# Optimization experiments

Measured on AMD Instinct MI355X. Metric: run time of the kernel, lower is better.

Reference implementation:

```python
import jax, jax.numpy as jnp
import numpy as np
from jax import lax

B, C, H, W = 1, 256, 64, 64
A = 9            # number of anchor sizes
STRIDE = 16      # base_stride
G = 28           # roi_grid_size
POOL = G // 2    # after 2x2 max pool -> 14
KPRE = 2000      # proposals entering NMS (obj_rank)
KPOST = 256      # RoIs kept after NMS
NCLS = 21        # head classes; head out dim = 5*NCLS
IOU_THR = 0.7


def _anchors():
    r = 2.0 ** 0.5
    out = []
    for b in (128.0, 256.0, 512.0):
        out += [(b, b), (b * r, b / r), (b / r, b * r)]
    return np.asarray(out, np.float32)  # [A,2] = (h, w)


def setup_inputs() -> dict:
    key = jax.random.key(0)
    ks = jax.random.split(key, 6)
    x = jax.random.normal(ks[0], (B, C, H, W), jnp.float32)
    rpn_w = jax.random.normal(ks[1], (256, C, 3, 3), jnp.float32) * 0.02
    rpn_b = jnp.zeros((256,), jnp.float32)
    cls_w = jax.random.normal(ks[2], (2 * A, 256), jnp.float32) * 0.05
    cls_b = jnp.zeros((2 * A,), jnp.float32)
    tfm_w = jax.random.normal(ks[3], (4 * A, 256), jnp.float32) * 0.01
    tfm_b = jnp.zeros((4 * A,), jnp.float32)
    head_w = jax.random.normal(ks[4], (5 * NCLS, C * POOL * POOL), jnp.float32) * 0.01
    head_b = jnp.zeros((5 * NCLS,), jnp.float32)
    anchors = jnp.asarray(_anchors())
    return dict(x=x, rpn_w=rpn_w, rpn_b=rpn_b, cls_w=cls_w, cls_b=cls_b,
                tfm_w=tfm_w, tfm_b=tfm_b, head_w=head_w, head_b=head_b,
                anchors=anchors)


def _forward(x, rpn_w, rpn_b, cls_w, cls_b, tfm_w, tfm_b, head_w, head_b, anchors):
    fm = x  # base == identity: input IS the backbone feature map [B,C,H,W]
    h = lax.conv_general_dilated(fm, rpn_w, (1, 1), 'SAME',
                                 dimension_numbers=('NCHW', 'OIHW', 'NCHW'))
    h = h + rpn_b[None, :, None, None]
    rpn_cls = jnp.einsum('oc,bchw->bohw', cls_w, h) + cls_b[None, :, None, None]
    rpn_tfm = jnp.einsum('oc,bchw->bohw', tfm_w, h) + tfm_b[None, :, None, None]

    # objectness: exp(pos)/(exp(pos)+exp(neg)) == sigmoid(pos-neg); channels interleaved
    obj = jax.nn.sigmoid(rpn_cls[:, 0::2] - rpn_cls[:, 1::2])  # [B,A,H,W]

    t = rpn_tfm.reshape(B, A, 4, H, W)
    aw = anchors[:, 1][None, :, None, None]
    ah = anchors[:, 0][None, :, None, None]
    jj = jnp.arange(W, dtype=jnp.float32)[None, None, None, :]
    ii = jnp.arange(H, dtype=jnp.float32)[None, None, :, None]
    bx = jj + aw * (t[:, :, 1] - 0.5) / STRIDE
    by = ii + ah * (t[:, :, 0] - 0.5) / STRIDE
    bw = aw / STRIDE * jnp.exp(t[:, :, 3])
    bh = ah / STRIDE * jnp.exp(t[:, :, 2])
    bx = jnp.clip(bx, 0.0, W - 1.0)
    by = jnp.clip(by, 0.0, H - 1.0)
    bw = jnp.clip(bx + bw, 0.0, W - 1.0) - bx
    bh = jnp.clip(by + bh, 0.0, H - 1.0) - by

    score = obj.reshape(-1)  # B==1, all scores > 0 (matches obj_score.nonzero())
    top_s, idx = lax.top_k(score, KPRE)  # sort descending (proposal ranking)
    # proposal path is computed under no_grad in the original
    top_s = lax.stop_gradient(top_s)
    bx, by, bw, bh = [lax.stop_gradient(v.reshape(-1)[idx]) for v in (bx, by, bw, bh)]

    # pairwise IoU on (x,y,w,h) boxes
    x2 = bx + bw; y2 = by + bh; area = bw * bh
    ix = jnp.maximum(bx[:, None], bx[None, :])
    iy = jnp.maximum(by[:, None], by[None, :])
    iw = jnp.clip(jnp.minimum(x2[:, None], x2[None, :]) - ix, 0.0)
    ih = jnp.clip(jnp.minimum(y2[:, None], y2[None, :]) - iy, 0.0)
    inter = iw * ih
    iou = inter / (area[:, None] + area[None, :] - inter)

    ar = jnp.arange(KPRE)
    def body(i, keep):  # greedy sequential NMS over score-sorted proposals
        sup = (iou[i] > IOU_THR) & (ar > i) & keep[i]
        return keep & (~sup)
    keep = lax.fori_loop(0, KPRE, body, jnp.ones((KPRE,), bool))

    _, sel = lax.top_k(jnp.where(keep, top_s, 0.0), KPOST)
    rx, ry, rw, rh = bx[sel], by[sel], bw[sel], bh[sel]  # feature-map coords

    fm0 = fm[0]  # [C,H,W]
    def align(px, py, pw, ph):
        # 28x28 bilinear sampling grid over the RoI, then 2x2 max pool -> 14x14
        gx = jnp.clip(px + (jnp.arange(G, dtype=jnp.float32) + 0.5) * pw / G, 0.0, W - 1.0)
        gy = jnp.clip(py + (jnp.arange(G, dtype=jnp.float32) + 0.5) * ph / G, 0.0, H - 1.0)
        x0 = jnp.clip(jnp.floor(gx), 0, W - 2).astype(jnp.int32)
        y0 = jnp.clip(jnp.floor(gy), 0, H - 2).astype(jnp.int32)
        wx = (gx - x0)[None, None, :]
        wy = (gy - y0)[None, :, None]
        f00 = fm0[:, y0[:, None], x0[None, :]]
        f01 = fm0[:, y0[:, None] + 1, x0[None, :]]
        f10 = fm0[:, y0[:, None], x0[None, :] + 1]
        f11 = fm0[:, y0[:, None] + 1, x0[None, :] + 1]
        out = (f00 * (1 - wy) * (1 - wx) + f01 * wy * (1 - wx)
               + f10 * (1 - wy) * wx + f11 * wy * wx)  # [C,G,G]
        return out.reshape(C, POOL, 2, POOL, 2).max(axis=(2, 4))

    feats = jax.vmap(align)(rx, ry, rw, rh)              # [KPOST,C,14,14]
    head_out = feats.reshape(KPOST, -1) @ head_w.T + head_b  # [KPOST,5*NCLS]
    final_cls = head_out[:, :NCLS]
    final_tfm = head_out[:, NCLS:]
    det = jnp.argmax(final_cls, axis=1)
    k = jnp.arange(KPOST)
    t0 = final_tfm[k, det * 4]
    t1 = final_tfm[k, det * 4 + 1]
    t2 = final_tfm[k, det * 4 + 2]
    t3 = final_tfm[k, det * 4 + 3]

    X = rx * STRIDE; Y = ry * STRIDE; Wd = rw * STRIDE; Hd = rh * STRIDE  # image coords
    fx = X + Wd * t1
    fy = Y + Hd * t0
    fw = Wd * jnp.exp(t3)
    fh = Hd * jnp.exp(t2)
    img = jnp.zeros((KPOST,), jnp.float32)
    final_bbox = jnp.stack([img, fx, fy, fw, fh], axis=1)
    proposal_bbox = jnp.stack([img, X, Y, Wd, Hd], axis=1)
    return rpn_cls, rpn_tfm, proposal_bbox, final_bbox, final_cls, final_tfm


def reference(x, rpn_w, rpn_b, cls_w, cls_b, tfm_w, tfm_b, head_w, head_b, anchors):
    return _forward(x, rpn_w, rpn_b, cls_w, cls_b, tfm_w, tfm_b, head_w, head_b, anchors)
```

## Files before the change

### kernel.cpp

```cpp
#include <hip/hip_runtime.h>
#include <math.h>

#define NPX   4096
#define NSC   36864
#define NKPRE 2000
#define NKPOST 256
#define GKS   98
#define CSPL  4

#define F_HPART  0
#define F_PART   0
#define F_H      4194304
#define F_FMT    5242880
#define F_XBH    6291456
#define F_XBL    6849024
#define F_WBH    7406592
#define F_WBL    7701504
#define F_FEATSB 6291456
#define F_HWB    12713984
#define F_UKEY   15523840
#define F_BX     15560704
#define F_BY     15597568
#define F_BW     15634432
#define F_BH     15671296
#define F_HIST   15708160
#define F_CAND   15773696
#define F_MASK   15781888
#define F_RBX    15909888
#define F_RBY    15911888
#define F_RBW    15913888
#define F_RBH    15915888
#define F_SEL    15917888
#define F_RXS    15918144
#define F_RYS    15918400
#define F_RWS    15918656
#define F_RHS    15918912
#define F_META   15919168
#define F_PRANK  15919184

typedef unsigned long long u64;
typedef unsigned int u32;
typedef unsigned short ushort;
typedef __attribute__((ext_vector_type(8))) short short8;
typedef __attribute__((ext_vector_type(4))) float floatx4;

__device__ __forceinline__ ushort f2bf(float f) {
    u32 b = __float_as_uint(f);
    b += 0x7FFFu + ((b >> 16) & 1u);
    return (ushort)(b >> 16);
}
__device__ __forceinline__ float bf2f(ushort h) {
    return __uint_as_float(((u32)h) << 16);
}
__device__ __forceinline__ u64 RL64(u64 v, int l) {
    u32 lo = (u32)__builtin_amdgcn_readlane((int)(u32)v, l);
    u32 hi = (u32)__builtin_amdgcn_readlane((int)(u32)(v >> 32), l);
    return ((u64)hi << 32) | lo;
}

__global__ void k_init(int* __restrict__ hist, int* __restrict__ meta,
                       int* __restrict__ prank) {
    int i = blockIdx.x * 256 + threadIdx.x;
    if (i < 65536) hist[i] = 0;
    if (i < 16) meta[i] = 0;
    if (i < 4096) prank[i] = 0;
}

__global__ void k_hwb(const float* __restrict__ head_w, ushort* __restrict__ hwb) {
    int e = (blockIdx.x * 256 + threadIdx.x) * 4;
    int o = e / 50176, k = e % 50176;
    ushort4 r;
    if (o < 105) {
        float4 v = *(const float4*)(head_w + (size_t)o * 50176 + k);
        r.x = f2bf(v.x); r.y = f2bf(v.y); r.z = f2bf(v.z); r.w = f2bf(v.w);
    } else {
        r.x = r.y = r.z = r.w = 0;
    }
    *(ushort4*)(hwb + (size_t)o * 50176 + k) = r;
}

__global__ void __launch_bounds__(256) k_transpose(const float* __restrict__ x,
                                                   float* __restrict__ fmt) {
    __shared__ float t[64][65];
    int pt = blockIdx.x;
    int ct = blockIdx.y;
    int tid = threadIdx.x;
    int px0 = pt * 64, c0 = ct * 64;
    int ln = tid & 63, sub = tid >> 6;
    for (int p = 0; p < 16; ++p) {
        int cl = p * 4 + sub;
        t[ln][cl] = x[(c0 + cl) * 4096 + px0 + ln];
    }
    __syncthreads();
    for (int p = 0; p < 16; ++p) {
        int pl = p * 4 + sub;
        fmt[(px0 + pl) * 256 + c0 + ln] = t[pl][ln];
    }
}

__global__ void k_xb(const float* __restrict__ fmt, ushort* __restrict__ xbh,
                     ushort* __restrict__ xbl) {
    int e = blockIdx.x * 256 + threadIdx.x;
    int p = e >> 6, cq = (e & 63) * 4;
    int yy = p / 66, xx = p % 66;
    float4 v = {0.f, 0.f, 0.f, 0.f};
    if (yy >= 1 && yy <= 64 && xx >= 1 && xx <= 64)
        v = *(const float4*)&fmt[((yy - 1) * 64 + (xx - 1)) * 256 + cq];
    ushort4 h, l;
    h.x = f2bf(v.x); l.x = f2bf(v.x - bf2f(h.x));
    h.y = f2bf(v.y); l.y = f2bf(v.y - bf2f(h.y));
    h.z = f2bf(v.z); l.z = f2bf(v.z - bf2f(h.z));
    h.w = f2bf(v.w); l.w = f2bf(v.w - bf2f(h.w));
    *(ushort4*)&xbh[(size_t)p * 256 + cq] = h;
    *(ushort4*)&xbl[(size_t)p * 256 + cq] = l;
}

__global__ void k_wb(const float* __restrict__ rpn_w, ushort* __restrict__ wbh,
                     ushort* __restrict__ wbl) {
    int e = blockIdx.x * 256 + threadIdx.x;
    int c = e & 255, oc = (e >> 8) & 255, t = e >> 16;
    float v = rpn_w[oc * 2304 + c * 9 + t];
    ushort h = f2bf(v);
    wbh[e] = h;
    wbl[e] = f2bf(v - bf2f(h));
}

__global__ void __launch_bounds__(256) k_conv(const ushort* __restrict__ xbh,
        const ushort* __restrict__ xbl, const ushort* __restrict__ wbh,
        const ushort* __restrict__ wbl, float* __restrict__ hpart) {
    __shared__ ushort lah[64 * 40], lal[64 * 40];
    __shared__ ushort lbh[64 * 40], lbl[64 * 40];
    int y0 = blockIdx.x;
    int oc0 = blockIdx.y * 64;
    int ksp = blockIdx.z;
    int tid = threadIdx.x;
    int wave = tid >> 6, lane = tid & 63;
    int m16 = lane & 15, quad = lane >> 4;
    floatx4 acc[4];
    #pragma unroll
    for (int nt = 0; nt < 4; ++nt) acc[nt] = (floatx4){0.f, 0.f, 0.f, 0.f};
    int sr = tid >> 2, sch = (tid & 3) * 8;
    for (int ki = ksp * 18; ki < ksp * 18 + 18; ++ki) {
        int t = ki >> 3, cb = ki & 7;
        int dy = t / 3, dx = t % 3;
        __syncthreads();
        {
            int rA0 = (y0 + dy) * 66 + dx;
            size_t g = (size_t)(rA0 + sr) * 256 + cb * 32 + sch;
            *(short8*)&lah[sr * 40 + sch] = *(const short8*)&xbh[g];
            *(short8*)&lal[sr * 40 + sch] = *(const short8*)&xbl[g];
        }
        {
            size_t g = (size_t)t * 65536 + (size_t)(oc0 + sr) * 256 + cb * 32 + sch;
            *(short8*)&lbh[sr * 40 + sch] = *(const short8*)&wbh[g];
            *(short8*)&lbl[sr * 40 + sch] = *(const short8*)&wbl[g];
        }
        __syncthreads();
        short8 ah = *(const short8*)&lah[(wave * 16 + m16) * 40 + quad * 8];
        short8 al = *(const short8*)&lal[(wave * 16 + m16) * 40 + quad * 8];
        #pragma unroll
        for (int nt = 0; nt < 4; ++nt) {
            short8 bh = *(const short8*)&lbh[(nt * 16 + m16) * 40 + quad * 8];
            short8 bl = *(const short8*)&lbl[(nt * 16 + m16) * 40 + quad * 8];
            acc[nt] = __builtin_amdgcn_mfma_f32_16x16x32_bf16(al, bh, acc[nt], 0, 0, 0);
            acc[nt] = __builtin_amdgcn_mfma_f32_16x16x32_bf16(ah, bl, acc[nt], 0, 0, 0);
            acc[nt] = __builtin_amdgcn_mfma_f32_16x16x32_bf16(ah, bh, acc[nt], 0, 0, 0);
        }
    }
    float* hp = hpart + (size_t)ksp * 1048576;
    #pragma unroll
    for (int nt = 0; nt < 4; ++nt) {
        int oc = oc0 + nt * 16 + m16;
        #pragma unroll
        for (int reg = 0; reg < 4; ++reg) {
            int px = y0 * 64 + wave * 16 + quad * 4 + reg;
            hp[oc * 4096 + px] = acc[nt][reg];
        }
    }
}

__global__ void k_convreduce(const float* __restrict__ hpart,
                             const float* __restrict__ rpn_b,
                             float* __restrict__ h) {
    int e = blockIdx.x * 256 + threadIdx.x;
    float s = 0.f;
    #pragma unroll
    for (int k = 0; k < CSPL; ++k) s += hpart[(size_t)k * 1048576 + e];
    h[e] = s + rpn_b[e >> 12];
}

__global__ void __launch_bounds__(256) k_heads(const float* __restrict__ h,
        const float* __restrict__ cls_w, const float* __restrict__ cls_b,
        const float* __restrict__ tfm_w, const float* __restrict__ tfm_b,
        const float* __restrict__ anchors,
        float* __restrict__ out_cls, float* __restrict__ out_tfm,
        u32* __restrict__ ukey, float* __restrict__ bxp, float* __restrict__ byp,
        float* __restrict__ bwp, float* __restrict__ bhp, int* __restrict__ hist) {
    __shared__ float w[256 * 56];
    __shared__ float ds[32 * 55];
    int tid = threadIdx.x;
    int px0 = blockIdx.x * 32;
    for (int e = tid; e < 54 * 256; e += 256) {
        int o = e >> 8, c = e & 255;
        float v = (o < 18) ? cls_w[o * 256 + c] : tfm_w[(o - 18) * 256 + c];
        w[c * 56 + o] = v;
    }
    __syncthreads();
    int ploc = tid & 31, og = tid >> 5;
    int px = px0 + ploc;
    float acc[7];
    #pragma unroll
    for (int j = 0; j < 7; ++j) acc[j] = 0.f;
    for (int c = 0; c < 256; ++c) {
        float hv = h[c * 4096 + px];
        #pragma unroll
        for (int j = 0; j < 7; ++j) acc[j] += hv * w[c * 56 + og * 7 + j];
    }
    #pragma unroll
    for (int j = 0; j < 7; ++j) {
        int o = og * 7 + j;
        if (o < 54) {
            float b = (o < 18) ? cls_b[o] : tfm_b[o - 18];
            float val = acc[j] + b;
            if (o < 18) out_cls[o * 4096 + px] = val;
            else        out_tfm[(o - 18) * 4096 + px] = val;
            ds[ploc * 55 + o] = val;
        }
    }
    __syncthreads();
    for (int t = tid; t < 288; t += 256) {
        int a = t >> 5, p = t & 31;
        int pxx = px0 + p;
        float pos = ds[p * 55 + 2 * a];
        float neg = ds[p * 55 + 2 * a + 1];
        float d = pos - neg;
        float sc = 1.f / (1.f + expf(-d));
        float t0 = ds[p * 55 + 18 + 4 * a + 0];
        float t1 = ds[p * 55 + 18 + 4 * a + 1];
        float t2 = ds[p * 55 + 18 + 4 * a + 2];
        float t3 = ds[p * 55 + 18 + 4 * a + 3];
        float ah = anchors[a * 2 + 0], aw = anchors[a * 2 + 1];
        float jx = (float)(pxx & 63), iy = (float)(pxx >> 6);
        float bx = jx + aw * (t1 - 0.5f) / 16.f;
        float by = iy + ah * (t0 - 0.5f) / 16.f;
        float bw = aw / 16.f * expf(t3);
        float bh = ah / 16.f * expf(t2);
        bx = fminf(fmaxf(bx, 0.f), 63.f);
        by = fminf(fmaxf(by, 0.f), 63.f);
        bw = fminf(fmaxf(bx + bw, 0.f), 63.f) - bx;
        bh = fminf(fmaxf(by + bh, 0.f), 63.f) - by;
        int idx = a * 4096 + pxx;
        u32 bits = __float_as_uint(sc);
        u32 u = (bits & 0x80000000u) ? ~bits : (bits ^ 0x80000000u);
        ukey[idx] = u;
        bxp[idx] = bx; byp[idx] = by; bwp[idx] = bw; bhp[idx] = bh;
        atomicAdd(&hist[u >> 16], 1);
    }
}

__global__ void __launch_bounds__(1024) k_scan(const int* __restrict__ hist,
                                               int* __restrict__ meta) {
    __shared__ int s[1024];
    int t = threadIdx.x;
    int base = 65536 - 64 * (t + 1);
    int sum = 0;
    for (int i = 0; i < 64; ++i) sum += hist[base + i];
    s[t] = sum;
    __syncthreads();
    int own = sum;
    for (int off = 1; off < 1024; off <<= 1) {
        int v = (t >= off) ? s[t - off] : 0;
        __syncthreads();
        s[t] += v;
        __syncthreads();
    }
    int cum = s[t], prev = cum - own;
    if (prev < NKPRE && cum >= NKPRE) {
        int c = prev;
        int b = 65535 - 64 * t;
        for (int i = 0; i < 64; ++i) {
            c += hist[b - i];
            if (c >= NKPRE) { meta[0] = b - i; break; }
        }
    }
}

__global__ void k_compact(const u32* __restrict__ ukey, const int* __restrict__ meta,
                          u64* __restrict__ cand, int* __restrict__ cnt) {
    int i = blockIdx.x * 256 + threadIdx.x;
    if (i >= NSC) return;
    u32 u = ukey[i];
    if ((int)(u >> 16) >= meta[0]) {
        int pos = atomicAdd(cnt, 1);
        if (pos < 4096) cand[pos] = (((u64)(~u)) << 32) | (u32)i;
    }
}

__global__ void __launch_bounds__(256) k_rank(const u64* __restrict__ cand,
                                              int* __restrict__ prank) {
    __shared__ u64 sk[256];
    int tid = threadIdx.x;
    int i = blockIdx.x * 256 + tid;
    int j0 = blockIdx.y * 256;
    sk[tid] = cand[j0 + tid];
    __syncthreads();
    u64 mykey = cand[i];
    int r = 0;
    #pragma unroll 8
    for (int j = 0; j < 256; j += 2) {
        ulonglong2 kv = *(const ulonglong2*)&sk[j];
        r += (kv.x < mykey) ? 1 : 0;
        r += (kv.y < mykey) ? 1 : 0;
    }
    atomicAdd(&prank[i], r);
}

__global__ void k_place(const u64* __restrict__ cand, const int* __restrict__ meta,
        const int* __restrict__ prank,
        const float* __restrict__ bxp, const float* __restrict__ byp,
        const float* __restrict__ bwp, const float* __restrict__ bhp,
        float* __restrict__ rbx, float* __restrict__ rby,
        float* __restrict__ rbw, float* __restrict__ rbh) {
    int i = blockIdx.x * 256 + threadIdx.x;
    int vc = meta[1]; if (vc > 4096) vc = 4096;
    if (i >= vc) return;
    int r = prank[i];
    if (r >= NKPRE) return;
    int idx = (int)(u32)(cand[i] & 0xFFFFFFFFULL);
    rbx[r] = bxp[idx]; rby[r] = byp[idx]; rbw[r] = bwp[idx]; rbh[r] = bhp[idx];
}

__global__ void __launch_bounds__(256) k_mask(const float* __restrict__ rbx,
        const float* __restrict__ rby, const float* __restrict__ rbw,
        const float* __restrict__ rbh, u64* __restrict__ mask) {
    int i = blockIdx.x;
    int lane = threadIdx.x & 63;
    int wave = threadIdx.x >> 6;
    float bxi = rbx[i], byi = rby[i], bwi = rbw[i], bhi = rbh[i];
    float x2i = bxi + bwi, y2i = byi + bhi, ari = bwi * bhi;
    for (int w = wave; w < 32; w += 4) {
        int j = w * 64 + lane;
        bool p = false;
        if (j < NKPRE && j > i) {
            float bxj = rbx[j], byj = rby[j], bwj = rbw[j], bhj = rbh[j];
            float x2j = bxj + bwj, y2j = byj + bhj, arj = bwj * bhj;
            float ix = fmaxf(bxi, bxj), iy = fmaxf(byi, byj);
            float iw = fmaxf(fminf(x2i, x2j) - ix, 0.f);
            float ih = fmaxf(fminf(y2i, y2j) - iy, 0.f);
            float inter = iw * ih;
            float iou = inter / (ari + arj - inter);
            p = iou > 0.7f;
        }
        u64 b = __ballot(p);
        if (lane == 0) mask[i * 32 + w] = b;
    }
}

__global__ void __launch_bounds__(64) k_nms(const u64* __restrict__ mask,
        const float* __restrict__ rbx, const float* __restrict__ rby,
        const float* __restrict__ rbw, const float* __restrict__ rbh,
        int* __restrict__ sel, float* __restrict__ rxs, float* __restrict__ rys,
        float* __restrict__ rws, float* __restrict__ rhs,
        u64* __restrict__ scratch) {
    __shared__ int klist[256];
    int lane = threadIdx.x;
    int lw = lane & 31;
    {
        const ulonglong2* m2 = (const ulonglong2*)mask;
        u64 acc = 0;
        #pragma unroll 25
        for (int it = lane; it < 32000; it += 64) {
            ulonglong2 v = m2[it];
            acc |= v.x | v.y;
        }
        scratch[lane] = acc;
    }
    u64 removed = 0ULL;
    int kcount = 0;
    u64 pf[32];
    #pragma unroll
    for (int s = 0; s < 32; ++s) pf[s] = mask[s * 32 + lw];
    bool done = false;
    for (int ib = 0; ib < NKPRE; ib += 32) {
        if (done) break;
        int cw = ib >> 6;
        int iw = (ib + 32) >> 6;
        u64 remC = RL64(removed, cw);
        u64 remI = RL64(removed, iw);
        #pragma unroll
        for (int s = 0; s < 32; ++s) {
            int ii = ib + s;
            u64 row = pf[s];
            int nx = ii + 32;
            if (!done && nx < NKPRE && !((remI >> (nx & 63)) & 1ULL))
                pf[s] = mask[(size_t)nx * 32 + lw];
            if (!done && ii < NKPRE && !((remC >> (ii & 63)) & 1ULL)) {
                if (lane == 0) klist[kcount] = ii;
                kcount++;
                if (lane < 32) removed |= row;
                remC |= RL64(row, cw);
                remI |= RL64(row, iw);
                if (kcount == NKPOST) done = true;
            }
        }
    }
    if (kcount < NKPOST) {
        for (int w = 0; w < 32 && kcount < NKPOST; ++w) {
            u64 wv = RL64(removed, w);
            int base = w << 6;
            for (int b = 0; b < 64; ++b) {
                int ii = base + b;
                if (ii >= NKPRE || kcount >= NKPOST) break;
                if ((wv >> b) & 1ULL) {
                    if (lane == 0) klist[kcount] = ii;
                    kcount++;
                }
            }
        }
    }
    __syncthreads();
    for (int s = lane; s < NKPOST; s += 64) {
        int id = klist[s];
        sel[s] = id;
        rxs[s] = rbx[id]; rys[s] = rby[id]; rws[s] = rbw[id]; rhs[s] = rbh[id];
    }
}

__global__ void __launch_bounds__(256) k_align(const float* __restrict__ fmt,
        const float* __restrict__ rxs, const float* __restrict__ rys,
        const float* __restrict__ rws, const float* __restrict__ rhs,
        ushort* __restrict__ feats) {
    __shared__ float buf[64 * 99];
    __shared__ int xs0[28], ys0[28];
    __shared__ float wxs[28], wys[28];
    int roi = blockIdx.x;
    int c0 = blockIdx.y * 64;
    int ch0 = blockIdx.z * 98;
    int tid = threadIdx.x;
    float rx = rxs[roi], ry = rys[roi], rw = rws[roi], rh = rhs[roi];
    if (tid < 28) {
        float g = rx + ((float)tid + 0.5f) * rw / 28.f;
        g = fminf(fmaxf(g, 0.f), 63.f);
        int x0 = (int)floorf(g); x0 = min(max(x0, 0), 62);
        xs0[tid] = x0; wxs[tid] = g - (float)x0;
        float g2 = ry + ((float)tid + 0.5f) * rh / 28.f;
        g2 = fminf(fmaxf(g2, 0.f), 63.f);
        int y0 = (int)floorf(g2); y0 = min(max(y0, 0), 62);
        ys0[tid] = y0; wys[tid] = g2 - (float)y0;
    }
    __syncthreads();
    int cl = tid & 63, cg = tid >> 6;
    for (int l = cg; l < 98; l += 4) {
        int cell = ch0 + l;
        int py = cell / 14, pxc = cell % 14;
        float m = -INFINITY;
        #pragma unroll
        for (int dy = 0; dy < 2; ++dy) {
            int sy = py * 2 + dy;
            int y0 = ys0[sy]; float wy = wys[sy];
            #pragma unroll
            for (int dx = 0; dx < 2; ++dx) {
                int sx = pxc * 2 + dx;
                int x0 = xs0[sx]; float wx = wxs[sx];
                int base = (y0 * 64 + x0) * 256 + c0 + cl;
                float f00 = fmt[base];
                float f10 = fmt[base + 256];
                float f01 = fmt[base + 64 * 256];
                float f11 = fmt[base + 64 * 256 + 256];
                float v = f00 * (1.f - wy) * (1.f - wx) + f01 * wy * (1.f - wx)
                        + f10 * (1.f - wy) * wx + f11 * wy * wx;
                m = fmaxf(m, v);
            }
        }
        buf[cl * 99 + l] = m;
    }
    __syncthreads();
    for (int e = tid; e < 64 * 98; e += 256) {
        int c = e / 98, l = e % 98;
        feats[(size_t)roi * 50176 + (c0 + c) * 196 + ch0 + l] = f2bf(buf[c * 99 + l]);
    }
}

__global__ void __launch_bounds__(256) k_gemm(const ushort* __restrict__ fb,
        const ushort* __restrict__ hwb, float* __restrict__ part) {
    int ks = blockIdx.x, rt = blockIdx.y;
    int wave = threadIdx.x >> 6, lane = threadIdx.x & 63;
    int m16 = lane & 15, quad = lane >> 4;
    int roiBase = rt * 64 + wave * 16;
    int kb = ks * 512;
    const ushort* arow = fb + (size_t)(roiBase + m16) * 50176 + kb + quad * 8;
    const ushort* brow = hwb + (size_t)m16 * 50176 + kb + quad * 8;
    floatx4 acc[7];
    #pragma unroll
    for (int t = 0; t < 7; ++t) acc[t] = (floatx4){0.f, 0.f, 0.f, 0.f};
    #pragma unroll 4
    for (int step = 0; step < 16; ++step) {
        short8 a = *(const short8*)(arow + step * 32);
        #pragma unroll
        for (int t = 0; t < 7; ++t) {
            short8 b = *(const short8*)(brow + (size_t)t * 16 * 50176 + step * 32);
            acc[t] = __builtin_amdgcn_mfma_f32_16x16x32_bf16(a, b, acc[t], 0, 0, 0);
        }
    }
    float* pbase = part + (size_t)ks * 26880;
    #pragma unroll
    for (int t = 0; t < 7; ++t) {
        int o = t * 16 + m16;
        if (o < 105) {
            #pragma unroll
            for (int reg = 0; reg < 4; ++reg) {
                int roi = roiBase + quad * 4 + reg;
                pbase[roi * 105 + o] = acc[t][reg];
            }
        }
    }
}

__global__ void k_reduce(const float* __restrict__ part, const float* __restrict__ head_b,
                         float* __restrict__ out_cls, float* __restrict__ out_tfm) {
    int e = blockIdx.x * 256 + threadIdx.x;
    if (e >= 26880) return;
    int roi = e / 105, o = e % 105;
    float s = 0.f;
    for (int ks = 0; ks < GKS; ++ks) s += part[(size_t)ks * 26880 + e];
    s += head_b[o];
    if (o < 21) out_cls[roi * 21 + o] = s;
    else        out_tfm[roi * 84 + (o - 21)] = s;
}

__global__ void __launch_bounds__(256) k_final(const float* __restrict__ out_cls,
        const float* __restrict__ out_tfm,
        const float* __restrict__ rxs, const float* __restrict__ rys,
        const float* __restrict__ rws, const float* __restrict__ rhs,
        float* __restrict__ prop, float* __restrict__ fbox) {
    int r = threadIdx.x;
    float best = out_cls[r * 21]; int det = 0;
    for (int o = 1; o < 21; ++o) {
        float v = out_cls[r * 21 + o];
        if (v > best) { best = v; det = o; }
    }
    float t0 = out_tfm[r * 84 + det * 4 + 0];
    float t1 = out_tfm[r * 84 + det * 4 + 1];
    float t2 = out_tfm[r * 84 + det * 4 + 2];
    float t3 = out_tfm[r * 84 + det * 4 + 3];
    float X = rxs[r] * 16.f, Y = rys[r] * 16.f, Wd = rws[r] * 16.f, Hd = rhs[r] * 16.f;
    float fx = X + Wd * t1, fy = Y + Hd * t0;
    float fw = Wd * expf(t3), fh = Hd * expf(t2);
    prop[r * 5 + 0] = 0.f; prop[r * 5 + 1] = X;  prop[r * 5 + 2] = Y;
    prop[r * 5 + 3] = Wd;  prop[r * 5 + 4] = Hd;
    fbox[r * 5 + 0] = 0.f; fbox[r * 5 + 1] = fx; fbox[r * 5 + 2] = fy;
    fbox[r * 5 + 3] = fw;  fbox[r * 5 + 4] = fh;
}

extern "C" void kernel_launch(void* const* d_in, const int* in_sizes, int n_in,
                              void* d_out, int out_size, void* d_ws, size_t ws_size,
                              hipStream_t stream) {
    const float* x      = (const float*)d_in[0];
    const float* rpn_w  = (const float*)d_in[1];
    const float* rpn_b  = (const float*)d_in[2];
    const float* cls_w  = (const float*)d_in[3];
    const float* cls_b  = (const float*)d_in[4];
    const float* tfm_w  = (const float*)d_in[5];
    const float* tfm_b  = (const float*)d_in[6];
    const float* head_w = (const float*)d_in[7];
    const float* head_b = (const float*)d_in[8];
    const float* anch   = (const float*)d_in[9];
    float* out = (float*)d_out;
    float* ws  = (float*)d_ws;

    float*  hpart  = ws + F_HPART;
    float*  h      = ws + F_H;
    float*  fmt    = ws + F_FMT;
    ushort* xbh    = (ushort*)(ws + F_XBH);
    ushort* xbl    = (ushort*)(ws + F_XBL);
    ushort* wbh    = (ushort*)(ws + F_WBH);
    ushort* wbl    = (ushort*)(ws + F_WBL);
    ushort* featsb = (ushort*)(ws + F_FEATSB);
    ushort* hwb    = (ushort*)(ws + F_HWB);
    float*  part   = ws + F_PART;
    u32*    ukey   = (u32*)(ws + F_UKEY);
    float*  bxp    = ws + F_BX;
    float*  byp    = ws + F_BY;
    float*  bwp    = ws + F_BW;
    float*  bhp    = ws + F_BH;
    int*    hist   = (int*)(ws + F_HIST);
    u64*    cand   = (u64*)(ws + F_CAND);
    u64*    mask   = (u64*)(ws + F_MASK);
    float*  rbx    = ws + F_RBX;
    float*  rby    = ws + F_RBY;
    float*  rbw    = ws + F_RBW;
    float*  rbh    = ws + F_RBH;
    int*    sel    = (int*)(ws + F_SEL);
    float*  rxs    = ws + F_RXS;
    float*  rys    = ws + F_RYS;
    float*  rws_p  = ws + F_RWS;
    float*  rhs_p  = ws + F_RHS;
    int*    meta   = (int*)(ws + F_META);
    int*    prank  = (int*)(ws + F_PRANK);

    float* out_rpncls = out + 0;
    float* out_rpntfm = out + 73728;
    float* out_prop   = out + 221184;
    float* out_fbox   = out + 222464;
    float* out_fcls   = out + 223744;
    float* out_ftfm   = out + 229120;

    k_init<<<256, 256, 0, stream>>>(hist, meta, prank);
    k_hwb<<<5488, 256, 0, stream>>>(head_w, hwb);
    k_transpose<<<dim3(64, 4), 256, 0, stream>>>(x, fmt);
    k_xb<<<1089, 256, 0, stream>>>(fmt, xbh, xbl);
    k_wb<<<2304, 256, 0, stream>>>(rpn_w, wbh, wbl);
    k_conv<<<dim3(64, 4, 4), 256, 0, stream>>>(xbh, xbl, wbh, wbl, hpart);
    k_convreduce<<<4096, 256, 0, stream>>>(hpart, rpn_b, h);
    k_heads<<<128, 256, 0, stream>>>(h, cls_w, cls_b, tfm_w, tfm_b, anch,
                                     out_rpncls, out_rpntfm, ukey, bxp, byp, bwp, bhp, hist);
    k_scan<<<1, 1024, 0, stream>>>(hist, meta);
    k_compact<<<144, 256, 0, stream>>>(ukey, meta, cand, meta + 1);
    k_rank<<<dim3(16, 16), 256, 0, stream>>>(cand, prank);
    k_place<<<16, 256, 0, stream>>>(cand, meta, prank, bxp, byp, bwp, bhp,
                                    rbx, rby, rbw, rbh);
    k_mask<<<2000, 256, 0, stream>>>(rbx, rby, rbw, rbh, mask);
    k_nms<<<1, 64, 0, stream>>>(mask, rbx, rby, rbw, rbh, sel, rxs, rys, rws_p, rhs_p,
                                cand);
    k_align<<<dim3(256, 4, 2), 256, 0, stream>>>(fmt, rxs, rys, rws_p, rhs_p, featsb);
    k_gemm<<<dim3(98, 4), 256, 0, stream>>>(featsb, hwb, part);
    k_reduce<<<105, 256, 0, stream>>>(part, head_b, out_fcls, out_ftfm);
    k_final<<<1, 256, 0, stream>>>(out_fcls, out_ftfm, rxs, rys, rws_p, rhs_p,
                                   out_prop, out_fbox);
}
```

Measured before the change: 343.8 us.

## Restructure NMS selection scan to per-64-box word processing with ctz iteration

Replaces the serial per-box greedy NMS scan, which kept 32 prefetched mask rows in registers and checked every box, with a per-64-box word loop. Each lane holds its diagonal mask word, the kept boxes inside a word are found by ctz iteration over the alive bits, and only kept rows are then loaded to update the removed set. The fill-up path for padding suppressed boxes now uses a wave-wide ballot-like popcount prefix instead of a serial bit loop. This cuts the iterations spent on suppressed boxes and the register pressure, but adds a readlane per kept box and serial dependent loads of kept rows.

```diff
diff --git a/kernel.cpp b/kernel.cpp
--- a/kernel.cpp
+++ b/kernel.cpp
@@ -377,45 +377,51 @@
     }
     u64 removed = 0ULL;
     int kcount = 0;
-    u64 pf[32];
-    #pragma unroll
-    for (int s = 0; s < 32; ++s) pf[s] = mask[s * 32 + lw];
+    u64 roww_cur = mask[(size_t)lane * 32 + 0];
     bool done = false;
-    for (int ib = 0; ib < NKPRE; ib += 32) {
-        if (done) break;
-        int cw = ib >> 6;
-        int iw = (ib + 32) >> 6;
-        u64 remC = RL64(removed, cw);
-        u64 remI = RL64(removed, iw);
-        #pragma unroll
-        for (int s = 0; s < 32; ++s) {
-            int ii = ib + s;
-            u64 row = pf[s];
-            int nx = ii + 32;
-            if (!done && nx < NKPRE && !((remI >> (nx & 63)) & 1ULL))
-                pf[s] = mask[(size_t)nx * 32 + lw];
-            if (!done && ii < NKPRE && !((remC >> (ii & 63)) & 1ULL)) {
-                if (lane == 0) klist[kcount] = ii;
-                kcount++;
-                if (lane < 32) removed |= row;
-                remC |= RL64(row, cw);
-                remI |= RL64(row, iw);
-                if (kcount == NKPOST) done = true;
-            }
-        }
+    for (int w = 0; w < 32 && !done; ++w) {
+        int base = w * 64;
+        int lim = NKPRE - base;
+        u64 limmask = (lim >= 64) ? ~0ULL : ((1ULL << lim) - 1ULL);
+        u64 roww_next = 0;
+        if (w + 1 < 32) {
+            int nb = (w + 1) * 64 + lane;
+            if (nb < NKPRE) roww_next = mask[(size_t)nb * 32 + (w + 1)];
+        }
+        u64 wrem = RL64(removed, w);
+        u64 alive = ~wrem & limmask;
+        u64 keptw = 0;
+        while (alive && !done) {
+            int b = __builtin_ctzll(alive);
+            if (lane == 0) klist[kcount] = base + b;
+            kcount++;
+            keptw |= (1ULL << b);
+            u64 rw = RL64(roww_cur, b);
+            alive &= ~rw;
+            alive &= ~(1ULL << b);
+            if (kcount == NKPOST) done = true;
+        }
+        u64 kk = keptw;
+        while (kk) {
+            int b = __builtin_ctzll(kk);
+            kk &= ~(1ULL << b);
+            u64 r = mask[(size_t)(base + b) * 32 + lw];
+            if (lane < 32) removed |= r;
+        }
+        roww_cur = roww_next;
     }
     if (kcount < NKPOST) {
         for (int w = 0; w < 32 && kcount < NKPOST; ++w) {
-            u64 wv = RL64(removed, w);
-            int base = w << 6;
-            for (int b = 0; b < 64; ++b) {
-                int ii = base + b;
-                if (ii >= NKPRE || kcount >= NKPOST) break;
-                if ((wv >> b) & 1ULL) {
-                    if (lane == 0) klist[kcount] = ii;
-                    kcount++;
-                }
+            int base = w * 64;
+            int lim = NKPRE - base;
+            u64 limmask = (lim >= 64) ? ~0ULL : ((1ULL << lim) - 1ULL);
+            u64 wv = RL64(removed, w) & limmask;
+            bool myset = (wv >> lane) & 1ULL;
+            if (myset) {
+                int pos = kcount + __builtin_popcountll(wv & ((1ULL << lane) - 1ULL));
+                if (pos < NKPOST) klist[pos] = base + lane;
             }
+            kcount += __builtin_popcountll(wv);
         }
     }
     __syncthreads();
```

New measurement: 359.6 us. 1.05x slower.
